# Performance work log

Hardware: AMD Instinct MI355X
Metric: run time of the kernel (lower is better)

The kernel has to match this reference:

```python
import jax, jax.numpy as jnp
import numpy as np

H8, W8 = 64, 64
H4, W4 = 128, 128
C_LAT, C_HI = 256, 128
N_Q = 1024
ORIG_H, ORIG_W = 512, 512
NUM_ITERS = 4
TEMP = 20.0
DIM = 4 + C_HI + C_LAT        # 388 mixer output dim
IN_DIM = DIM + 3 * 49         # 535 mixer input dim
HID = 512


def _unit(v):
    return v / jnp.sqrt(jnp.maximum(jnp.sum(v * v, axis=-1, keepdims=True), 1e-12))


def setup_inputs() -> dict:
    key = jax.random.key(0)
    ks = jax.random.split(key, 20)
    fg = _unit(jax.random.normal(ks[0], (1, H8, W8, C_LAT), jnp.float32))
    hg = _unit(jax.random.normal(ks[1], (1, H4, W4, C_HI), jnp.float32))
    qf = _unit(jax.random.normal(ks[2], (1, N_Q, C_LAT), jnp.float32))
    hq = _unit(jax.random.normal(ks[3], (1, N_Q, C_HI), jnp.float32))
    p = lambda k, s, sc=0.05: sc * jax.random.normal(k, s, jnp.float32)
    return dict(
        feature_grid=fg, hires_feats_grid=hg, query_feats=qf, hires_query_feats=hq,
        hid1_w=p(ks[4], (16, 1, 3, 3)), hid1_b=jnp.zeros((16,), jnp.float32),
        hid2_w=p(ks[5], (1, 16, 3, 3)), hid2_b=jnp.zeros((1,), jnp.float32),
        hid3_w=p(ks[6], (32, 16, 3, 3)), hid3_b=jnp.zeros((32,), jnp.float32),
        hid4_w=p(ks[7], (32, 16)), hid4_b=jnp.zeros((16,), jnp.float32),
        occ_w=p(ks[8], (16, 2)), occ_b=jnp.zeros((2,), jnp.float32),
        mix_in_w=p(ks[9], (IN_DIM, HID), 0.02), mix_in_b=jnp.zeros((HID,), jnp.float32),
        mix_out_w=p(ks[10], (HID, DIM), 0.02), mix_out_b=jnp.zeros((DIM,), jnp.float32),
    )


def _conv2d(x, w, b, stride, pad):
    y = jax.lax.conv_general_dilated(x, w, (stride, stride), pad,
                                     dimension_numbers=('NCHW', 'OIHW', 'NCHW'))
    return y + b[None, :, None, None]


def _bilinear_sample(grid, coords):
    # grid [H,W,C]; coords [..., 2] as (y, x); edge-clamped bilinear gather.
    H, W = grid.shape[0], grid.shape[1]
    y, x = coords[..., 0], coords[..., 1]
    y0f, x0f = jnp.floor(y), jnp.floor(x)
    wy, wx = (y - y0f)[..., None], (x - x0f)[..., None]
    y0 = jnp.clip(y0f.astype(jnp.int32), 0, H - 1)
    y1 = jnp.clip(y0f.astype(jnp.int32) + 1, 0, H - 1)
    x0 = jnp.clip(x0f.astype(jnp.int32), 0, W - 1)
    x1 = jnp.clip(x0f.astype(jnp.int32) + 1, 0, W - 1)
    g00, g01 = grid[y0, x0], grid[y0, x1]
    g10, g11 = grid[y1, x0], grid[y1, x1]
    return (g00 * (1 - wy) * (1 - wx) + g01 * (1 - wy) * wx
            + g10 * wy * (1 - wx) + g11 * wy * wx)


def _forward(fg, hg, qf, hq, hid1_w, hid1_b, hid2_w, hid2_b, hid3_w, hid3_b,
             hid4_w, hid4_b, occ_w, occ_b, mix_in_w, mix_in_b, mix_out_w, mix_out_b):
    # --- tracks_from_cost_volume ---
    cv = jnp.einsum('bnc,bhwc->bnhw', qf, fg)                 # [1,N,64,64]
    b, n, h, w = cv.shape
    x = cv.reshape(b * n, 1, h, w)
    occ_map = jax.nn.relu(_conv2d(x, hid1_w, hid1_b, 1, 'SAME'))   # [bn,16,h,w]
    pmap = _conv2d(occ_map, hid2_w, hid2_b, 1, 'SAME').reshape(b * n, h * w)
    heat = jax.nn.softmax(pmap * TEMP, axis=-1).reshape(b * n, h, w)
    ey = jnp.einsum('bhw,h->b', heat, jnp.arange(h, dtype=jnp.float32))
    ex = jnp.einsum('bhw,w->b', heat, jnp.arange(w, dtype=jnp.float32))
    points = jnp.stack([ex * (ORIG_W / w), ey * (ORIG_H / h)], -1).reshape(b, n, 2)
    op = jnp.pad(occ_map, ((0, 0), (0, 0), (0, 2), (0, 2)))
    o3 = jax.nn.relu(_conv2d(op, hid3_w, hid3_b, 2, 'VALID'))
    o3 = o3.mean((-1, -2))                                     # [bn,32]
    o3 = jax.nn.relu(o3 @ hid4_w + hid4_b)
    o3 = (o3 @ occ_w + occ_b).reshape(b, n, 2)
    occ, expd = o3[..., 0], o3[..., 1]

    # --- iterative pips refinement ---
    cy, cx = jnp.meshgrid(jnp.arange(-3, 4), jnp.arange(-3, 4), indexing='ij')
    ctx = jnp.stack([cy, cx], -1).reshape(-1, 2).astype(jnp.float32)   # [49,2] (dy,dx)
    fg_avg = fg.reshape(1, H8 // 2, 2, W8 // 2, 2, C_LAT).mean((2, 4))
    pyramid = [hg, fg, fg_avg]
    feats = jnp.concatenate([hq, qf], -1)                      # [1,N,384]
    pos = points
    for it in range(NUM_ITERS):
        if it == 0:
            queries = [hq[0], qf[0], qf[0]]
        else:
            queries = [feats[0, :, :C_HI], feats[0, :, C_HI:], feats[0, :, C_HI:]]
        corrs = []
        for grid, q in zip(pyramid, queries):
            gh, gw = grid.shape[1], grid.shape[2]
            scale = jnp.array([gw / ORIG_W, gh / ORIG_H], jnp.float32)
            c = (pos[0] * scale)[:, ::-1]                      # (x,y)->(y,x), [N,2]
            coords2 = c[:, None, :] + ctx[None]                # [N,49,2]
            nb = _bilinear_sample(grid[0], coords2)            # [N,49,C]
            corrs.append(jnp.einsum('nsc,nc->ns', nb, q))
        corrs = jnp.concatenate(corrs, -1)[None]               # [1,N,147]
        mlp_in = jnp.concatenate([jnp.zeros_like(pos), occ[..., None],
                                  expd[..., None], feats, corrs], -1)
        res = jax.nn.gelu(mlp_in @ mix_in_w + mix_in_b) @ mix_out_w + mix_out_b
        pos = pos + res[..., :2]
        occ = occ + res[..., 2]
        expd = expd + res[..., 3]
        feats = feats + res[..., 4:]
    return jnp.concatenate([pos, occ[..., None], expd[..., None]], -1)  # [1,N,4]


def reference(feature_grid, hires_feats_grid, query_feats, hires_query_feats,
              hid1_w, hid1_b, hid2_w, hid2_b, hid3_w, hid3_b, hid4_w, hid4_b,
              occ_w, occ_b, mix_in_w, mix_in_b, mix_out_w, mix_out_b):
    return _forward(feature_grid, hires_feats_grid, query_feats, hires_query_feats,
                    hid1_w, hid1_b, hid2_w, hid2_b, hid3_w, hid3_b, hid4_w, hid4_b,
                    occ_w, occ_b, mix_in_w, mix_in_b, mix_out_w, mix_out_b)
```

## Files before the change

### kernel.cpp

```cpp
#include <hip/hip_runtime.h>
#include <hip/hip_bf16.h>
#include <math.h>


#define NQ 1024
#define TEMPF 20.0f
#define DIMV 388
#define INDIM 535
#define KPAD 544
#define HID 512

#define WS_CVB     0
#define WS_WIT     2097152
#define WS_WOT     2236416
#define WS_FG16    2351104
#define WS_HG16    2875392
#define WS_AV16    3923968
#define WS_FGAVG   4194304
#define WS_POS     (WS_FGAVG + 262144)
#define WS_OCC     (WS_POS + NQ*2)
#define WS_EXPD    (WS_OCC + NQ)
#define WS_FEATS   (WS_EXPD + NQ)
#define WS_MLPIN   (WS_FEATS + NQ*384)
#define WS_HIDDEN  (WS_MLPIN + NQ*KPAD)
#define WS_W3B     (WS_HIDDEN + NQ*HID)
#define WS_PART    (WS_MLPIN + 278528)
#define WS_SUM3    WS_HIDDEN

#define OP 72
#define CVP 68

typedef __attribute__((ext_vector_type(8))) short bf16x8;
typedef __attribute__((ext_vector_type(4))) float f32x4;

union BU8 { uint4 u; __hip_bfloat16 h[8]; };

__global__ __launch_bounds__(256) void k_prep_cv(
    const float* __restrict__ fg, const float* __restrict__ qf,
    const float* __restrict__ hq, const float* __restrict__ w3,
    float* __restrict__ ws) {
  __shared__ __hip_bfloat16 A_s[32 * 32];
  __shared__ __hip_bfloat16 B_s[64 * 32];
  const int bx = blockIdx.x;
  const int t = threadIdx.x;

  if (bx >= 2048) {
    int i = (bx - 2048) * 256 + t;
    if (i < 262144) {
      int c = i & 255, ox = (i >> 8) & 31, oy = i >> 13;
      const float* b = fg + (((oy * 2) * 64 + ox * 2) << 8) + c;
      ws[WS_FGAVG + i] = 0.25f * (b[0] + b[256] + b[16384] + b[16384 + 256]);
    } else if (i < 262144 + 393216) {
      int j = i - 262144;
      int n = j / 384, c = j - n * 384;
      float v = (c < 128) ? hq[n * 128 + c] : qf[n * 256 + c - 128];
      ws[WS_FEATS + j] = v;
      __hip_bfloat16* mi = (__hip_bfloat16*)(ws + WS_MLPIN);
      mi[n * KPAD + 4 + c] = __float2bfloat16(v);
      if (c == 0) {
        mi[n * KPAD + 0] = __float2bfloat16(0.f);
        mi[n * KPAD + 1] = __float2bfloat16(0.f);
      }
    } else if (i < 262144 + 393216 + 5120) {
      int j = i - (262144 + 393216);
      int e = j & 7, qd = (j >> 3) & 3, nl = (j >> 5) & 15;
      int nt = (j >> 9) & 1, kt = j >> 10;
      int k = kt * 32 + qd * 8 + e;
      int ic = k & 15, tap = k >> 4;
      int oc = nt * 16 + nl;
      float v = (tap < 9) ? w3[(oc * 16 + ic) * 9 + tap] : 0.f;
      ((__hip_bfloat16*)(ws + WS_W3B))[j] = __float2bfloat16(v);
    } else if (i < 262144 + 393216 + 5120 + 524288) {
      int j = i - (262144 + 393216 + 5120);
      ws[WS_SUM3 + j] = 0.f;
    }
    return;
  }

  const int wv = t >> 6, lane = t & 63;
  const int wm = wv & 1, wn = wv >> 1;
  const int quad = lane >> 4, nl = lane & 15;
  const int p0 = (bx & 63) * 64, m0 = (bx >> 6) * 32;
  f32x4 acc0 = {0.f, 0.f, 0.f, 0.f};
  f32x4 acc1 = {0.f, 0.f, 0.f, 0.f};

  for (int k0 = 0; k0 < 256; k0 += 32) {
    {
      int r = t >> 3, c = t & 7;
      float4 v = *(const float4*)&qf[(m0 + r) * 256 + k0 + c * 4];
      union { __hip_bfloat16 h[4]; uint2 u; } pk;
      pk.h[0] = __float2bfloat16(v.x); pk.h[1] = __float2bfloat16(v.y);
      pk.h[2] = __float2bfloat16(v.z); pk.h[3] = __float2bfloat16(v.w);
      *(uint2*)&A_s[r * 32 + c * 4] = pk.u;
    }
    {
      int r = t >> 2, c = t & 3;
      const float* src = &fg[(p0 + r) * 256 + k0 + c * 8];
      float4 v0 = *(const float4*)src;
      float4 v1 = *(const float4*)(src + 4);
      union { __hip_bfloat16 h[8]; uint4 u; } pk;
      pk.h[0] = __float2bfloat16(v0.x); pk.h[1] = __float2bfloat16(v0.y);
      pk.h[2] = __float2bfloat16(v0.z); pk.h[3] = __float2bfloat16(v0.w);
      pk.h[4] = __float2bfloat16(v1.x); pk.h[5] = __float2bfloat16(v1.y);
      pk.h[6] = __float2bfloat16(v1.z); pk.h[7] = __float2bfloat16(v1.w);
      *(uint4*)&B_s[r * 32 + c * 8] = pk.u;
    }
    __syncthreads();
    bf16x8 a = *(const bf16x8*)&A_s[(16 * wm + nl) * 32 + quad * 8];
    bf16x8 b0 = *(const bf16x8*)&B_s[(32 * wn + nl) * 32 + quad * 8];
    bf16x8 b1 = *(const bf16x8*)&B_s[(32 * wn + 16 + nl) * 32 + quad * 8];
    acc0 = __builtin_amdgcn_mfma_f32_16x16x32_bf16(a, b0, acc0, 0, 0, 0);
    acc1 = __builtin_amdgcn_mfma_f32_16x16x32_bf16(a, b1, acc1, 0, 0, 0);
    __syncthreads();
  }
  __hip_bfloat16* cvb = (__hip_bfloat16*)ws;
#pragma unroll
  for (int nt = 0; nt < 2; nt++) {
    int n = p0 + 32 * wn + nt * 16 + nl;
#pragma unroll
    for (int r = 0; r < 4; r++) {
      int m = m0 + 16 * wm + quad * 4 + r;
      cvb[m * 4096 + n] = __float2bfloat16(nt ? acc1[r] : acc0[r]);
    }
  }
}

__global__ __launch_bounds__(256, 5) void k_head_stripe(
    const float* __restrict__ h1w, const float* __restrict__ h1b,
    const float* __restrict__ h2w, const float* __restrict__ h2b,
    const float* __restrict__ h3b, float* __restrict__ ws) {
  __shared__ float cvs[8 * CVP];
  __shared__ float occ[6 * 16 * OP];

  const int bx = blockIdx.x;
  const int q = bx >> 4, st = bx & 15;
  const int y0 = st * 4;
  const int t = threadIdx.x;
  const int wv = t >> 6, lane = t & 63;
  const int role = (wv + bx) & 3;
  const __hip_bfloat16* cvb = (const __hip_bfloat16*)ws + q * 4096;

  if (t < 192) {
    int rc = t >> 1, side = t & 1;
    *(float4*)&occ[rc * OP + side * 68] = make_float4(0.f, 0.f, 0.f, 0.f);
  }
  if (st == 0 || st == 15) {
    int r = (st == 0) ? 0 : 5;
    for (int i = t; i < 16 * 18; i += 256)
      *(float4*)&occ[(r * 16 + (i / 18)) * OP + (i % 18) * 4] =
          make_float4(0.f, 0.f, 0.f, 0.f);
  }
#pragma unroll
  for (int j = 0; j < 2; j++) {
    int i = t + 256 * j;
    int lr = i >> 6, x = i & 63;
    int g = y0 - 2 + lr;
    cvs[lr * CVP + x + 1] =
        (g >= 0 && g < 64) ? __bfloat162float(cvb[g * 64 + x]) : 0.f;
  }
  if (t < 32) {
    int rr = t >> 2, c = t & 3;
    cvs[rr * CVP + ((c == 0) ? 0 : (64 + c))] = 0.f;
  }
  __syncthreads();

  {
    const int x = lane;
    const int chg = wv * 4;
    float w1r[4][9], b1r[4];
#pragma unroll
    for (int k = 0; k < 4; k++) {
      b1r[k] = h1b[chg + k];
#pragma unroll
      for (int j = 0; j < 9; j++) w1r[k][j] = h1w[(chg + k) * 9 + j];
    }
    float win[3][3];
#pragma unroll
    for (int j = 0; j < 3; j++) {
      const float* cp = &cvs[j * CVP + x];
      win[j][0] = cp[0]; win[j][1] = cp[1]; win[j][2] = cp[2];
    }
    for (int r = 0; r < 6; r++) {
      if (r > 0) {
#pragma unroll
        for (int c = 0; c < 3; c++) { win[0][c] = win[1][c]; win[1][c] = win[2][c]; }
        const float* cp = &cvs[(r + 2) * CVP + x];
        win[2][0] = cp[0]; win[2][1] = cp[1]; win[2][2] = cp[2];
      }
      int yo = y0 - 1 + r;
      if (yo >= 0 && yo <= 63) {
#pragma unroll
        for (int k = 0; k < 4; k++) {
          float a = b1r[k];
#pragma unroll
          for (int ky = 0; ky < 3; ky++)
            a += w1r[k][3 * ky] * win[ky][0] + w1r[k][3 * ky + 1] * win[ky][1] +
                 w1r[k][3 * ky + 2] * win[ky][2];
          occ[(r * 16 + chg + k) * OP + x + 4] = fmaxf(a, 0.f);
        }
      }
    }
  }
  __syncthreads();

  if (role == 1 || role == 2) {
    const __hip_bfloat16* W3B = (const __hip_bfloat16*)(ws + WS_W3B);
    const int oyl = role - 1;
    const int nl = lane & 15;
    const int qd = lane >> 4, qh = qd >> 1, ql = qd & 1;
    f32x4 acc00 = {0.f,0.f,0.f,0.f}, acc01 = {0.f,0.f,0.f,0.f};
    f32x4 acc10 = {0.f,0.f,0.f,0.f}, acc11 = {0.f,0.f,0.f,0.f};
#pragma unroll
    for (int kt = 0; kt < 5; kt++) {
      int tap = kt * 2 + qh;
      int tv = (tap < 9) ? tap : 0;
      int ky = (tv >= 6) ? 2 : ((tv >= 3) ? 1 : 0);
      int kx = tv - 3 * ky;
      const float* ap =
          &occ[((2 * oyl + 1 + ky) * 16 + ql * 8) * OP + 4 + kx + 2 * nl];
      union { bf16x8 v; __hip_bfloat16 h[8]; } a0u, a1u;
      if (tap < 9) {
#pragma unroll
        for (int j = 0; j < 8; j++) {
          a0u.h[j] = __float2bfloat16(ap[j * OP]);
          a1u.h[j] = __float2bfloat16(ap[j * OP + 32]);
        }
      } else {
#pragma unroll
        for (int j = 0; j < 8; j++) {
          a0u.h[j] = __float2bfloat16(0.f);
          a1u.h[j] = __float2bfloat16(0.f);
        }
      }
      bf16x8 b0 = *(const bf16x8*)&W3B[((kt * 2 + 0) * 16 + nl) * 32 + qd * 8];
      bf16x8 b1 = *(const bf16x8*)&W3B[((kt * 2 + 1) * 16 + nl) * 32 + qd * 8];
      acc00 = __builtin_amdgcn_mfma_f32_16x16x32_bf16(a0u.v, b0, acc00, 0, 0, 0);
      acc01 = __builtin_amdgcn_mfma_f32_16x16x32_bf16(a0u.v, b1, acc01, 0, 0, 0);
      acc10 = __builtin_amdgcn_mfma_f32_16x16x32_bf16(a1u.v, b0, acc10, 0, 0, 0);
      acc11 = __builtin_amdgcn_mfma_f32_16x16x32_bf16(a1u.v, b1, acc11, 0, 0, 0);
    }
    float bb0 = h3b[nl], bb1 = h3b[16 + nl];
    float s0 = 0.f, s1 = 0.f;
#pragma unroll
    for (int r = 0; r < 4; r++) {
      s0 += fmaxf(acc00[r] + bb0, 0.f) + fmaxf(acc10[r] + bb0, 0.f);
      s1 += fmaxf(acc01[r] + bb1, 0.f) + fmaxf(acc11[r] + bb1, 0.f);
    }
    s0 += __shfl_xor(s0, 16); s0 += __shfl_xor(s0, 32);
    s1 += __shfl_xor(s1, 16); s1 += __shfl_xor(s1, 32);
    if (lane < 16) {
      atomicAdd(&ws[WS_SUM3 + (q * 16 + st) * 32 + nl], s0);
      atomicAdd(&ws[WS_SUM3 + (q * 16 + st) * 32 + 16 + nl], s1);
    }
  } else {
    const int rl = ((role == 3) ? 2 : 0) + (lane >> 5);
    const int yg = y0 + rl;
    const int x0 = (lane & 31) * 2;
    float pa = 0.f, pb = 0.f;
    for (int ch = 0; ch < 16; ch++) {
#pragma unroll
      for (int ky = 0; ky < 3; ky++) {
        const float* bp = &occ[((rl + ky) * 16 + ch) * OP + x0];
        float f0 = bp[3];
        float2 fm = *(const float2*)(bp + 4);
        float f3 = bp[6];
        float wa = h2w[ch * 9 + 3 * ky], wb = h2w[ch * 9 + 3 * ky + 1],
              wc = h2w[ch * 9 + 3 * ky + 2];
        pa += wa * f0 + wb * fm.x + wc * fm.y;
        pb += wa * fm.x + wb * fm.y + wc * f3;
      }
    }
    float bb = h2b[0];
    float v0 = (pa + bb) * TEMPF, v1 = (pb + bb) * TEMPF;
    float mg = fmaxf(v0, v1);
#pragma unroll
    for (int off = 1; off < 64; off <<= 1) mg = fmaxf(mg, __shfl_xor(mg, off));
    float e0 = __expf(v0 - mg), e1 = __expf(v1 - mg);
    float s = e0 + e1;
    float sx = e0 * (float)x0 + e1 * (float)(x0 + 1);
    float sy = s * (float)yg;
#pragma unroll
    for (int off = 1; off < 64; off <<= 1) {
      s += __shfl_xor(s, off);
      sx += __shfl_xor(sx, off);
      sy += __shfl_xor(sy, off);
    }
    if (lane == 0) {
      int slot = q * 32 + st * 2 + ((role == 3) ? 1 : 0);
      *(float4*)&ws[WS_PART + slot * 4] = make_float4(mg, s, sx, sy);
    }
  }
}

__global__ __launch_bounds__(256) void k_merge_cvt(
    const float* __restrict__ w4, const float* __restrict__ b4,
    const float* __restrict__ w5, const float* __restrict__ b5,
    const float* __restrict__ wi, const float* __restrict__ wo,
    const float* __restrict__ fg, const float* __restrict__ hg,
    float* __restrict__ ws) {
  {
    int i = blockIdx.x * 256 + threadIdx.x;
    __hip_bfloat16* WIT = (__hip_bfloat16*)(ws + WS_WIT);
    __hip_bfloat16* WOT = (__hip_bfloat16*)(ws + WS_WOT);
    if (i < 278528) {
      int n = i / KPAD, k = i - n * KPAD;
      float v = (k < INDIM) ? wi[k * HID + n] : 0.f;
      WIT[i] = __float2bfloat16(v);
    } else if (i < 507904) {
      int j = i - 278528;
      int n = j >> 9, k = j & 511;
      float v = (n < DIMV) ? wo[k * DIMV + n] : 0.f;
      WOT[j] = __float2bfloat16(v);
    } else {
      int j = i - 507904;
      if (j < 1048576) {
        ((__hip_bfloat16*)(ws + WS_FG16))[j] = __float2bfloat16(fg[j]);
      } else if (j < 3145728) {
        int k = j - 1048576;
        ((__hip_bfloat16*)(ws + WS_HG16))[k] = __float2bfloat16(hg[k]);
      } else if (j < 3407872) {
        int k = j - 3145728;
        ((__hip_bfloat16*)(ws + WS_AV16))[k] = __float2bfloat16(ws[WS_FGAVG + k]);
      }
    }
  }
  if (blockIdx.x >= 256) return;

  __shared__ float sums_s[4][32];
  __shared__ float o4s[4][16];
  int t = threadIdx.x, wv = t >> 6, lane = t & 63;
  int q = blockIdx.x * 4 + wv;

  float M = -1e30f, S = 0.f, SX = 0.f, SY = 0.f;
  if (lane < 32) {
    float4 pv = *(const float4*)&ws[WS_PART + (q * 32 + lane) * 4];
    M = pv.x; S = pv.y; SX = pv.z; SY = pv.w;
  }
#pragma unroll
  for (int off = 1; off < 64; off <<= 1) {
    float Mo = __shfl_xor(M, off), So = __shfl_xor(S, off);
    float SXo = __shfl_xor(SX, off), SYo = __shfl_xor(SY, off);
    float Mn = fmaxf(M, Mo);
    float c1 = __expf(M - Mn), c2 = __expf(Mo - Mn);
    S = S * c1 + So * c2; SX = SX * c1 + SXo * c2; SY = SY * c1 + SYo * c2;
    M = Mn;
  }
  if (lane == 0) {
    ws[WS_POS + q * 2 + 0] = (SX / S) * 8.0f;
    ws[WS_POS + q * 2 + 1] = (SY / S) * 8.0f;
  }

  int ch = lane & 31, half = lane >> 5;
  float sm = 0.f;
#pragma unroll
  for (int s8 = 0; s8 < 8; s8++)
    sm += ws[WS_SUM3 + (q * 16 + half * 8 + s8) * 32 + ch];
  sm += __shfl_xor(sm, 32);
  if (lane < 32) sums_s[wv][lane] = sm * (1.f / 1024.f);
  __syncthreads();
  if (lane < 16) {
    float a = b4[lane];
#pragma unroll
    for (int i = 0; i < 32; i++) a += sums_s[wv][i] * w4[i * 16 + lane];
    o4s[wv][lane] = fmaxf(a, 0.f);
  }
  __syncthreads();
  if (lane < 2) {
    float r = b5[lane];
#pragma unroll
    for (int j = 0; j < 16; j++) r += o4s[wv][j] * w5[j * 2 + lane];
    __hip_bfloat16* mi = (__hip_bfloat16*)(ws + WS_MLPIN);
    if (lane == 0) { ws[WS_OCC + q] = r;  mi[q * KPAD + 2] = __float2bfloat16(r); }
    else           { ws[WS_EXPD + q] = r; mi[q * KPAD + 3] = __float2bfloat16(r); }
  }
}

__global__ __launch_bounds__(256) void k_corr(float* __restrict__ ws) {
  __shared__ float qs[384];
  __shared__ float dbuf[3][64];
  int t = threadIdx.x;
  int wv = t >> 6, lane = t & 63;
  int cl = lane & 15, sub = lane >> 4;
  int n = blockIdx.x;
  const float* feats = ws + WS_FEATS + n * 384;
  float posx = ws[WS_POS + n * 2 + 0];
  float posy = ws[WS_POS + n * 2 + 1];
  __hip_bfloat16* mi = (__hip_bfloat16*)(ws + WS_MLPIN) + n * KPAD;

  for (int col = t; col < 384; col += 256) qs[col] = feats[col];
  __syncthreads();

  float qh[8], qq[16];
#pragma unroll
  for (int j = 0; j < 8; j++) qh[j] = qs[cl * 8 + j];
#pragma unroll
  for (int j = 0; j < 16; j++) qq[j] = qs[128 + cl * 16 + j];

  const __hip_bfloat16* G0 = (const __hip_bfloat16*)(ws + WS_HG16);
  const __hip_bfloat16* G1 = (const __hip_bfloat16*)(ws + WS_FG16);
  const __hip_bfloat16* G2 = (const __hip_bfloat16*)(ws + WS_AV16);

#pragma unroll
  for (int L = 0; L < 3; L++) {
    const __hip_bfloat16* grid;
    int Hg, Wg;
    float scl;
    if (L == 0)      { grid = G0; Hg = 128; Wg = 128; scl = 0.25f; }
    else if (L == 1) { grid = G1; Hg = 64;  Wg = 64;  scl = 0.125f; }
    else             { grid = G2; Hg = 32;  Wg = 32;  scl = 0.0625f; }
    float cy = posy * scl, cx = posx * scl;
    int iy = (int)floorf(cy), ix = (int)floorf(cx);
#pragma unroll
    for (int g = 0; g < 4; g++) {
      int p = wv * 16 + g * 4 + sub;
      int a = p >> 3, b = p & 7;
      int row = iy + a - 3; row = row < 0 ? 0 : (row > Hg - 1 ? Hg - 1 : row);
      int col = ix + b - 3; col = col < 0 ? 0 : (col > Wg - 1 ? Wg - 1 : col);
      float acc = 0.f;
      if (L == 0) {
        BU8 g0; g0.u = *(const uint4*)(grid + (row * Wg + col) * 128 + cl * 8);
#pragma unroll
        for (int j = 0; j < 8; j++) acc += __bfloat162float(g0.h[j]) * qh[j];
      } else {
        const __hip_bfloat16* gp = grid + (row * Wg + col) * 256 + cl * 16;
        BU8 g0, g1;
        g0.u = *(const uint4*)gp;
        g1.u = *(const uint4*)(gp + 8);
#pragma unroll
        for (int j = 0; j < 8; j++) {
          acc += __bfloat162float(g0.h[j]) * qq[j];
          acc += __bfloat162float(g1.h[j]) * qq[8 + j];
        }
      }
      acc += __shfl_xor(acc, 1);
      acc += __shfl_xor(acc, 2);
      acc += __shfl_xor(acc, 4);
      acc += __shfl_xor(acc, 8);
      if (cl == 0) dbuf[L][p] = acc;
    }
  }
  __syncthreads();

  if (t < 147) {
    int L = t / 49, s = t - L * 49;
    int sa = s / 7, sb = s - sa * 7;
    float scl = (L == 0) ? 0.25f : ((L == 1) ? 0.125f : 0.0625f);
    float cy = posy * scl, cx = posx * scl;
    float wy = cy - floorf(cy), wx = cx - floorf(cx);
    int i00 = sa * 8 + sb;
    float d00 = dbuf[L][i00], d01 = dbuf[L][i00 + 1];
    float d10 = dbuf[L][i00 + 8], d11 = dbuf[L][i00 + 9];
    float corr = (1.f - wy) * (1.f - wx) * d00 + (1.f - wy) * wx * d01 +
                 wy * (1.f - wx) * d10 + wy * wx * d11;
    mi[388 + t] = __float2bfloat16(corr);
  }
}

__device__ __forceinline__ float gelu_tanh(float x) {
  float z = 0.7978845608028654f * (x + 0.044715f * x * x * x);
  z = fminf(fmaxf(z, -15.f), 15.f);
  float e = __expf(2.f * z);
  float th = (e - 1.f) / (e + 1.f);
  return 0.5f * x * (1.f + th);
}

__global__ __launch_bounds__(256) void k_mix1(
    const float* __restrict__ bias, float* __restrict__ ws) {
  const int t = threadIdx.x;
  const int wv = t >> 6, lane = t & 63;
  const int nt = blockIdx.x * 4 + wv;
  const int mt = blockIdx.y;
  const int m0 = mt * 16, n0 = nt * 16;
  const int nl = lane & 15, quad = lane >> 4;
  const unsigned short* Abf = (const unsigned short*)(ws + WS_MLPIN);
  const unsigned short* WIT = (const unsigned short*)(ws + WS_WIT);
  const unsigned short* ap = &Abf[(m0 + nl) * KPAD + quad * 8];
  const unsigned short* bp = &WIT[(n0 + nl) * KPAD + quad * 8];
  f32x4 acc = {0.f, 0.f, 0.f, 0.f};
#pragma unroll
  for (int ks = 0; ks < 17; ks++) {
    bf16x8 a = *(const bf16x8*)(ap + ks * 32);
    bf16x8 b = *(const bf16x8*)(bp + ks * 32);
    acc = __builtin_amdgcn_mfma_f32_16x16x32_bf16(a, b, acc, 0, 0, 0);
  }
  __hip_bfloat16* Hd = (__hip_bfloat16*)(ws + WS_HIDDEN);
  int nn = n0 + nl;
  float bv = bias[nn];
#pragma unroll
  for (int r = 0; r < 4; r++) {
    int m = m0 + quad * 4 + r;
    Hd[m * HID + nn] = __float2bfloat16(gelu_tanh(acc[r] + bv));
  }
}

__global__ __launch_bounds__(256) void k_mix2(
    const float* __restrict__ bias, float* __restrict__ ws,
    float* __restrict__ out) {
  const int t = threadIdx.x;
  const int wv = t >> 6, lane = t & 63;
  const int nt = blockIdx.x * 4 + wv;
  const int mt = blockIdx.y;
  const int m0 = mt * 16, n0 = nt * 16;
  const int nl = lane & 15, quad = lane >> 4;
  const unsigned short* Abf = (const unsigned short*)(ws + WS_HIDDEN);
  const unsigned short* WOT = (const unsigned short*)(ws + WS_WOT);
  const unsigned short* ap = &Abf[(m0 + nl) * HID + quad * 8];
  const unsigned short* bp = &WOT[(n0 + nl) * HID + quad * 8];
  f32x4 acc = {0.f, 0.f, 0.f, 0.f};
#pragma unroll
  for (int ks = 0; ks < 16; ks++) {
    bf16x8 a = *(const bf16x8*)(ap + ks * 32);
    bf16x8 b = *(const bf16x8*)(bp + ks * 32);
    acc = __builtin_amdgcn_mfma_f32_16x16x32_bf16(a, b, acc, 0, 0, 0);
  }

  int col = n0 + nl;
  if (col < DIMV) {
    float bv = bias[col];
    __hip_bfloat16* mib = (__hip_bfloat16*)(ws + WS_MLPIN);
#pragma unroll
    for (int r = 0; r < 4; r++) {
      int m = m0 + quad * 4 + r;
      float rr = acc[r] + bv;
      if (col < 2) {
        float v = ws[WS_POS + m * 2 + col] + rr;
        ws[WS_POS + m * 2 + col] = v;
        out[m * 4 + col] = v;
      } else if (col == 2) {
        float v = ws[WS_OCC + m] + rr;
        ws[WS_OCC + m] = v;
        out[m * 4 + 2] = v;
        mib[m * KPAD + 2] = __float2bfloat16(v);
      } else if (col == 3) {
        float v = ws[WS_EXPD + m] + rr;
        ws[WS_EXPD + m] = v;
        out[m * 4 + 3] = v;
        mib[m * KPAD + 3] = __float2bfloat16(v);
      } else {
        float v = ws[WS_FEATS + m * 384 + (col - 4)] + rr;
        ws[WS_FEATS + m * 384 + (col - 4)] = v;
        mib[m * KPAD + col] = __float2bfloat16(v);
      }
    }
  }
}

extern "C" void kernel_launch(void* const* d_in, const int* in_sizes, int n_in,
                              void* d_out, int out_size, void* d_ws, size_t ws_size,
                              hipStream_t stream) {
  const float* fg = (const float*)d_in[0];
  const float* hg = (const float*)d_in[1];
  const float* qf = (const float*)d_in[2];
  const float* hq = (const float*)d_in[3];
  const float* w1 = (const float*)d_in[4];
  const float* b1 = (const float*)d_in[5];
  const float* w2 = (const float*)d_in[6];
  const float* b2 = (const float*)d_in[7];
  const float* w3 = (const float*)d_in[8];
  const float* b3 = (const float*)d_in[9];
  const float* w4 = (const float*)d_in[10];
  const float* b4 = (const float*)d_in[11];
  const float* w5 = (const float*)d_in[12];
  const float* b5 = (const float*)d_in[13];
  const float* wi = (const float*)d_in[14];
  const float* bi = (const float*)d_in[15];
  const float* wo = (const float*)d_in[16];
  const float* bo = (const float*)d_in[17];
  float* ws = (float*)d_ws;
  float* out = (float*)d_out;

  k_prep_cv<<<6676, 256, 0, stream>>>(fg, qf, hq, w3, ws);
  k_head_stripe<<<16384, 256, 0, stream>>>(w1, b1, w2, b2, b3, ws);
  k_merge_cvt<<<15296, 256, 0, stream>>>(w4, b4, w5, b5, wi, wo, fg, hg, ws);
  for (int it = 0; it < 4; it++) {
    k_corr<<<1024, 256, 0, stream>>>(ws);
    k_mix1<<<dim3(8, 64), 256, 0, stream>>>(bi, ws);
    k_mix2<<<dim3(7, 64), 256, 0, stream>>>(bo, ws, out);
  }
}
```

Baseline: 309.0 us.

## Move weight and grid bf16 conversions into prep kernel with vectorized writes

Moves the mixer weight transposes and the feature/hires grid bf16 conversions out of the merge kernel into the prep kernel, and vectorizes the grid conversions as float4 loads with packed bf16 stores. The pooled feature average is written straight to bf16, which drops the fp32 intermediate and its re-read. The merge kernel now launches only its 256 real blocks instead of a large mostly-conversion grid. The occupancy stripe also changes to interleaved column ownership (x and x+32) for coalesced LDS reads, at the cost of a larger prep grid.

After: 309.9 us. About the same (+0.3%).

```diff
diff --git a/kernel.cpp b/kernel.cpp
--- a/kernel.cpp
+++ b/kernel.cpp
@@ -36,9 +36,10 @@
 union BU8 { uint4 u; __hip_bfloat16 h[8]; };
 
 __global__ __launch_bounds__(256) void k_prep_cv(
-    const float* __restrict__ fg, const float* __restrict__ qf,
-    const float* __restrict__ hq, const float* __restrict__ w3,
-    float* __restrict__ ws) {
+    const float* __restrict__ fg, const float* __restrict__ hg,
+    const float* __restrict__ qf, const float* __restrict__ hq,
+    const float* __restrict__ w3, const float* __restrict__ wi,
+    const float* __restrict__ wo, float* __restrict__ ws) {
   __shared__ __hip_bfloat16 A_s[32 * 32];
   __shared__ __hip_bfloat16 B_s[64 * 32];
   const int bx = blockIdx.x;
@@ -49,8 +50,9 @@
     if (i < 262144) {
       int c = i & 255, ox = (i >> 8) & 31, oy = i >> 13;
       const float* b = fg + (((oy * 2) * 64 + ox * 2) << 8) + c;
-      ws[WS_FGAVG + i] = 0.25f * (b[0] + b[256] + b[16384] + b[16384 + 256]);
-    } else if (i < 262144 + 393216) {
+      float av = 0.25f * (b[0] + b[256] + b[16384] + b[16384 + 256]);
+      ((__hip_bfloat16*)(ws + WS_AV16))[i] = __float2bfloat16(av);
+    } else if (i < 655360) {
       int j = i - 262144;
       int n = j / 384, c = j - n * 384;
       float v = (c < 128) ? hq[n * 128 + c] : qf[n * 256 + c - 128];
@@ -61,8 +63,8 @@
         mi[n * KPAD + 0] = __float2bfloat16(0.f);
         mi[n * KPAD + 1] = __float2bfloat16(0.f);
       }
-    } else if (i < 262144 + 393216 + 5120) {
-      int j = i - (262144 + 393216);
+    } else if (i < 660480) {
+      int j = i - 655360;
       int e = j & 7, qd = (j >> 3) & 3, nl = (j >> 5) & 15;
       int nt = (j >> 9) & 1, kt = j >> 10;
       int k = kt * 32 + qd * 8 + e;
@@ -70,9 +72,32 @@
       int oc = nt * 16 + nl;
       float v = (tap < 9) ? w3[(oc * 16 + ic) * 9 + tap] : 0.f;
       ((__hip_bfloat16*)(ws + WS_W3B))[j] = __float2bfloat16(v);
-    } else if (i < 262144 + 393216 + 5120 + 524288) {
-      int j = i - (262144 + 393216 + 5120);
-      ws[WS_SUM3 + j] = 0.f;
+    } else if (i < 1184768) {
+      ws[WS_SUM3 + (i - 660480)] = 0.f;
+    } else if (i < 1463296) {
+      int j = i - 1184768;
+      int n = j / KPAD, k = j - n * KPAD;
+      float v = (k < INDIM) ? wi[k * HID + n] : 0.f;
+      ((__hip_bfloat16*)(ws + WS_WIT))[j] = __float2bfloat16(v);
+    } else if (i < 1692672) {
+      int j = i - 1463296;
+      int n = j >> 9, k = j & 511;
+      float v = (n < DIMV) ? wo[k * DIMV + n] : 0.f;
+      ((__hip_bfloat16*)(ws + WS_WOT))[j] = __float2bfloat16(v);
+    } else if (i < 1954816) {
+      int j = (i - 1692672) * 4;
+      float4 v = *(const float4*)&fg[j];
+      union { __hip_bfloat16 h[4]; uint2 u; } pk;
+      pk.h[0] = __float2bfloat16(v.x); pk.h[1] = __float2bfloat16(v.y);
+      pk.h[2] = __float2bfloat16(v.z); pk.h[3] = __float2bfloat16(v.w);
+      *(uint2*)(((__hip_bfloat16*)(ws + WS_FG16)) + j) = pk.u;
+    } else {
+      int j = (i - 1954816) * 4;
+      float4 v = *(const float4*)&hg[j];
+      union { __hip_bfloat16 h[4]; uint2 u; } pk;
+      pk.h[0] = __float2bfloat16(v.x); pk.h[1] = __float2bfloat16(v.y);
+      pk.h[2] = __float2bfloat16(v.z); pk.h[3] = __float2bfloat16(v.w);
+      *(uint2*)(((__hip_bfloat16*)(ws + WS_HG16)) + j) = pk.u;
     }
     return;
   }
@@ -255,19 +280,17 @@
   } else {
     const int rl = ((role == 3) ? 2 : 0) + (lane >> 5);
     const int yg = y0 + rl;
-    const int x0 = (lane & 31) * 2;
+    const int xa = lane & 31;
+    const int xb = xa + 32;
     float pa = 0.f, pb = 0.f;
     for (int ch = 0; ch < 16; ch++) {
 #pragma unroll
       for (int ky = 0; ky < 3; ky++) {
-        const float* bp = &occ[((rl + ky) * 16 + ch) * OP + x0];
-        float f0 = bp[3];
-        float2 fm = *(const float2*)(bp + 4);
-        float f3 = bp[6];
+        const float* bp = &occ[((rl + ky) * 16 + ch) * OP];
         float wa = h2w[ch * 9 + 3 * ky], wb = h2w[ch * 9 + 3 * ky + 1],
               wc = h2w[ch * 9 + 3 * ky + 2];
-        pa += wa * f0 + wb * fm.x + wc * fm.y;
-        pb += wa * fm.x + wb * fm.y + wc * f3;
+        pa += wa * bp[xa + 3] + wb * bp[xa + 4] + wc * bp[xa + 5];
+        pb += wa * bp[xb + 3] + wb * bp[xb + 4] + wc * bp[xb + 5];
       }
     }
     float bb = h2b[0];
@@ -277,7 +300,7 @@
     for (int off = 1; off < 64; off <<= 1) mg = fmaxf(mg, __shfl_xor(mg, off));
     float e0 = __expf(v0 - mg), e1 = __expf(v1 - mg);
     float s = e0 + e1;
-    float sx = e0 * (float)x0 + e1 * (float)(x0 + 1);
+    float sx = e0 * (float)xa + e1 * (float)xb;
     float sy = s * (float)yg;
 #pragma unroll
     for (int off = 1; off < 64; off <<= 1) {
@@ -292,40 +315,10 @@
   }
 }
 
-__global__ __launch_bounds__(256) void k_merge_cvt(
+__global__ __launch_bounds__(256) void k_merge(
     const float* __restrict__ w4, const float* __restrict__ b4,
     const float* __restrict__ w5, const float* __restrict__ b5,
-    const float* __restrict__ wi, const float* __restrict__ wo,
-    const float* __restrict__ fg, const float* __restrict__ hg,
     float* __restrict__ ws) {
-  {
-    int i = blockIdx.x * 256 + threadIdx.x;
-    __hip_bfloat16* WIT = (__hip_bfloat16*)(ws + WS_WIT);
-    __hip_bfloat16* WOT = (__hip_bfloat16*)(ws + WS_WOT);
-    if (i < 278528) {
-      int n = i / KPAD, k = i - n * KPAD;
-      float v = (k < INDIM) ? wi[k * HID + n] : 0.f;
-      WIT[i] = __float2bfloat16(v);
-    } else if (i < 507904) {
-      int j = i - 278528;
-      int n = j >> 9, k = j & 511;
-      float v = (n < DIMV) ? wo[k * DIMV + n] : 0.f;
-      WOT[j] = __float2bfloat16(v);
-    } else {
-      int j = i - 507904;
-      if (j < 1048576) {
-        ((__hip_bfloat16*)(ws + WS_FG16))[j] = __float2bfloat16(fg[j]);
-      } else if (j < 3145728) {
-        int k = j - 1048576;
-        ((__hip_bfloat16*)(ws + WS_HG16))[k] = __float2bfloat16(hg[k]);
-      } else if (j < 3407872) {
-        int k = j - 3145728;
-        ((__hip_bfloat16*)(ws + WS_AV16))[k] = __float2bfloat16(ws[WS_FGAVG + k]);
-      }
-    }
-  }
-  if (blockIdx.x >= 256) return;
-
   __shared__ float sums_s[4][32];
   __shared__ float o4s[4][16];
   int t = threadIdx.x, wv = t >> 6, lane = t & 63;
@@ -569,9 +562,9 @@
   float* ws = (float*)d_ws;
   float* out = (float*)d_out;
 
-  k_prep_cv<<<6676, 256, 0, stream>>>(fg, qf, hq, w3, ws);
+  k_prep_cv<<<11732, 256, 0, stream>>>(fg, hg, qf, hq, w3, wi, wo, ws);
   k_head_stripe<<<16384, 256, 0, stream>>>(w1, b1, w2, b2, b3, ws);
-  k_merge_cvt<<<15296, 256, 0, stream>>>(w4, b4, w5, b5, wi, wo, fg, hg, ws);
+  k_merge<<<256, 256, 0, stream>>>(w4, b4, w5, b5, ws);
   for (int it = 0; it < 4; it++) {
     k_corr<<<1024, 256, 0, stream>>>(ws);
     k_mix1<<<dim3(8, 64), 256, 0, stream>>>(bi, ws);
```
